# Kernel optimization log

Measured on AMD Instinct MI355X. Metric: run time of the kernel, lower is better.

The kernel has to match this reference:

```python
import jax, jax.numpy as jnp
import numpy as np

# --- config (matches init_kwargs) ---
HID = 2048      # hidden_size
H = 16          # num_attention_heads
D_NOPE = 128    # qk_nope_head_dim
D_ROPE = 64     # qk_rope_head_dim
D_Q = D_NOPE + D_ROPE  # 192
D_V = 128       # v_head_dim
QR = 1536       # q_lora_rank
KVR = 512       # kv_lora_rank
PH = 16         # pattern_heads
PD = HID // PH  # 128
THETA = 10000.0
EPS = 1e-6


def rmsnorm(x, w):
    var = jnp.mean(jnp.square(x), axis=-1, keepdims=True)
    return x * jax.lax.rsqrt(var + EPS) * w


def rope_cos_sin(seq_len):
    inv_freq = 1.0 / (THETA ** (jnp.arange(0, D_ROPE, 2, dtype=jnp.float32) / D_ROPE))
    t = jnp.arange(seq_len, dtype=jnp.float32)
    freqs = jnp.outer(t, inv_freq)            # [S, D_ROPE/2]
    emb = jnp.concatenate([freqs, freqs], -1)  # [S, D_ROPE]
    return jnp.cos(emb), jnp.sin(emb)


def rotate_half(x):
    x1, x2 = jnp.split(x, 2, axis=-1)
    return jnp.concatenate([-x2, x1], axis=-1)


def apply_rope(x, cos, sin):
    # x: [B, H, S, D_ROPE]; cos/sin: [S, D_ROPE]
    return x * cos[None, None] + rotate_half(x) * sin[None, None]


def setup_inputs() -> dict:
    key = jax.random.key(0)
    ks = jax.random.split(key, 12)
    def w(k, shape):
        return (jax.random.normal(k, shape, jnp.float32) / np.sqrt(shape[-1])).astype(jnp.float32)
    B, S = 2, 1024
    return {
        "hidden_states": jax.random.normal(ks[0], (B, S, HID), jnp.float32),
        "q_a_w": w(ks[1], (QR, HID)),
        "q_a_ln_w": jnp.ones((QR,), jnp.float32),
        "q_b_w": w(ks[2], (H * D_Q, QR)),
        "kv_a_w": w(ks[3], (KVR + H * D_ROPE, HID)),
        "kv_a_ln_w": jnp.ones((KVR,), jnp.float32),
        "kv_b_w": w(ks[4], (H * (D_NOPE + D_V), KVR)),
        "o_w": w(ks[5], (HID, H * D_V)),
        "sp_q_w": w(ks[6], (HID, HID)),
        "sp_k_w": w(ks[7], (HID, HID)),
        "sp_v_w": w(ks[8], (HID, HID)),
        "sp_o_w": w(ks[9], (HID, HID)),
        "gate_w": w(ks[10], (2, HID)),
        "gate_b": jnp.zeros((2,), jnp.float32),
    }


def reference(hidden_states, q_a_w, q_a_ln_w, q_b_w, kv_a_w, kv_a_ln_w, kv_b_w,
              o_w, sp_q_w, sp_k_w, sp_v_w, sp_o_w, gate_w, gate_b):
    b, s, _ = hidden_states.shape
    dt = hidden_states.dtype

    # ---- main MLA path ----
    q_mid = rmsnorm(hidden_states @ q_a_w.T, q_a_ln_w)                      # [B,S,QR]
    q = (q_mid @ q_b_w.T).reshape(b, s, H, D_Q).transpose(0, 2, 1, 3)       # [B,H,S,Dq]
    q_nope, q_pe = q[..., :D_NOPE], q[..., D_NOPE:]

    kv_a = hidden_states @ kv_a_w.T                                         # [B,S,KVR+H*Dr]
    kv_lora, k_pe_flat = kv_a[..., :KVR], kv_a[..., KVR:]
    k_pe = k_pe_flat.reshape(b, s, H, D_ROPE).transpose(0, 2, 1, 3)         # [B,H,S,Dr]

    kv = (rmsnorm(kv_lora, kv_a_ln_w) @ kv_b_w.T)
    kv = kv.reshape(b, s, H, D_NOPE + D_V).transpose(0, 2, 1, 3)            # [B,H,S,Dn+Dv]
    k_nope, v = kv[..., :D_NOPE], kv[..., D_NOPE:]

    cos, sin = rope_cos_sin(s)
    q_pe = apply_rope(q_pe, cos, sin)
    k_pe = apply_rope(k_pe, cos, sin)

    qf = jnp.concatenate([q_nope, q_pe], -1)                                # [B,H,S,Dq]
    kf = jnp.concatenate([k_nope, k_pe], -1)

    scale = D_Q ** -0.5
    scores = jnp.einsum('bhqd,bhkd->bhqk', qf, kf) * scale
    probs = jax.nn.softmax(scores.astype(jnp.float32), axis=-1).astype(dt)
    ctx = jnp.einsum('bhqk,bhkd->bhqd', probs, v)                           # [B,H,S,Dv]
    main_out = ctx.transpose(0, 2, 1, 3).reshape(b, s, H * D_V) @ o_w.T     # [B,S,HID]

    # ---- self pattern path (standard MHA on hidden_states) ----
    def split_heads(x):
        return x.reshape(b, s, PH, PD).transpose(0, 2, 1, 3)
    pq = split_heads(hidden_states @ sp_q_w.T)
    pk = split_heads(hidden_states @ sp_k_w.T)
    pv = split_heads(hidden_states @ sp_v_w.T)
    p_scores = jnp.einsum('bhqd,bhkd->bhqk', pq, pk) * (PD ** -0.5)
    p_probs = jax.nn.softmax(p_scores.astype(jnp.float32), axis=-1).astype(dt)
    p_ctx = jnp.einsum('bhqk,bhkd->bhqd', p_probs, pv)
    pattern_out = p_ctx.transpose(0, 2, 1, 3).reshape(b, s, HID) @ sp_o_w.T

    # ---- learned gate over paths ----
    gates = jax.nn.softmax(hidden_states @ gate_w.T + gate_b, axis=-1)      # [B,S,2]
    return gates[..., 0:1] * main_out + gates[..., 1:2] * pattern_out
```

## Files before the change

kernel.cpp:

```cpp
#include <hip/hip_runtime.h>
#include <math.h>
#include <stdint.h>

#define HIDN  2048
#define NH    16
#define DNOPE 128
#define DROPE 64
#define DQ    192
#define DV    128
#define QRANK 1536
#define KVRANK 512
#define SEQ   1024
#define NBATCH 2
#define NTOK  (NBATCH*SEQ)
#define EPSV  1e-6f

typedef unsigned short u16;
typedef unsigned int   u32;
typedef __attribute__((ext_vector_type(8))) short  short8;
typedef __attribute__((ext_vector_type(8))) unsigned short ushort8;
typedef __attribute__((ext_vector_type(4))) float  f32x4;

__device__ __forceinline__ u16 f2b(float f) {
    u32 u = __float_as_uint(f);
    u = (u + 0x7fffu + ((u >> 16) & 1u)) >> 16;
    return (u16)u;
}
__device__ __forceinline__ float b2f(u16 h) {
    return __uint_as_float(((u32)h) << 16);
}

__device__ __forceinline__ void async_copy16(const u16* g, u16* l) {
    __builtin_amdgcn_global_load_lds(
        (const __attribute__((address_space(1))) u32*)g,
        (__attribute__((address_space(3))) u32*)l,
        16, 0, 0);
}

__device__ __forceinline__ int swz(int r, int c) { return r * 4 + (c ^ ((r >> 1) & 3)); }

struct CastArgs {
    const float* s[10];
    u16* d[10];
    int cum[11];
};
__global__ __launch_bounds__(256)
void cast_all(CastArgs a, int total_chunks)
{
    int c = blockIdx.x * 256 + threadIdx.x;
    if (c >= total_chunks) return;
    int seg = 0;
    #pragma unroll
    for (int i = 1; i < 10; ++i) seg += (c >= a.cum[i]) ? 1 : 0;
    int local = c - a.cum[seg];
    const float* src = a.s[seg] + (size_t)local * 8;
    u16* dst = a.d[seg] + (size_t)local * 8;
    float4 x = *(const float4*)(src);
    float4 y = *(const float4*)(src + 4);
    ushort8 o;
    o[0]=f2b(x.x); o[1]=f2b(x.y); o[2]=f2b(x.z); o[3]=f2b(x.w);
    o[4]=f2b(y.x); o[5]=f2b(y.y); o[6]=f2b(y.z); o[7]=f2b(y.w);
    *(ushort8*)(dst) = o;
}

struct GemmSeg {
    const u16* X; const u16* W;
    float* Cf; u16* Cb; u16* Cb2; u16* Cb3;
    int K; int ldx; int ldc; int mode; int bx0;
};
struct GemmArgs { GemmSeg seg[3]; int nseg; };

__global__ __launch_bounds__(256)
void gemm_multi(GemmArgs a)
{
    __shared__ __align__(16) u16 As[2 * 4096];
    __shared__ __align__(16) u16 Bs[2 * 4096];
    int s = 0;
    if (a.nseg > 1 && (int)blockIdx.x >= a.seg[1].bx0) s = 1;
    if (a.nseg > 2 && (int)blockIdx.x >= a.seg[2].bx0) s = 2;
    const GemmSeg g = a.seg[s];

    const int tid = threadIdx.x;
    const int bn = ((int)blockIdx.x - g.bx0) * 128;
    const int bm = blockIdx.y * 128;
    const int lane = tid & 63, wv = tid >> 6;
    const int lm = lane & 15, lq = lane >> 4;
    const int wm = (wv >> 1) * 64, wn = (wv & 1) * 64;
    const int ldx = g.ldx, K = g.K;
    const u16* Xp = g.X;
    const u16* Wp = g.W;

    auto stage = [&](int kt, int buf) {
        int k0 = kt * 32;
        #pragma unroll
        for (int it = 0; it < 2; ++it) {
            int base = wv * 64 + it * 256;
            int slot = base + lane;
            int r = slot >> 2, c = (slot & 3) ^ ((r >> 1) & 3);
            async_copy16(Xp + (size_t)(bm + r) * ldx + k0 + c * 8,
                         As + buf * 4096 + base * 8);
            async_copy16(Wp + (size_t)(bn + r) * K + k0 + c * 8,
                         Bs + buf * 4096 + base * 8);
        }
    };

    f32x4 acc[4][4] = {};
    const int niter = K >> 5;
    stage(0, 0);
    for (int kt = 0; kt < niter; ++kt) {
        int cur = kt & 1;
        __syncthreads();
        if (kt + 1 < niter) stage(kt + 1, cur ^ 1);
        const u16* Ab = As + cur * 4096;
        const u16* Bb = Bs + cur * 4096;
        short8 af[4], bf[4];
        #pragma unroll
        for (int mt = 0; mt < 4; ++mt) {
            int R = wm + mt * 16 + lm;
            af[mt] = *(const short8*)(Ab + swz(R, lq) * 8);
        }
        #pragma unroll
        for (int nt = 0; nt < 4; ++nt) {
            int R = wn + nt * 16 + lm;
            bf[nt] = *(const short8*)(Bb + swz(R, lq) * 8);
        }
        #pragma unroll
        for (int mt = 0; mt < 4; ++mt)
            #pragma unroll
            for (int nt = 0; nt < 4; ++nt)
                acc[mt][nt] = __builtin_amdgcn_mfma_f32_16x16x32_bf16(
                    af[mt], bf[nt], acc[mt][nt], 0, 0, 0);
    }

    const int mode = g.mode;
    #pragma unroll
    for (int mt = 0; mt < 4; ++mt) {
        int token0 = bm + wm + mt * 16 + lq * 4;
        #pragma unroll
        for (int nt = 0; nt < 4; ++nt) {
            int feat = bn + wn + nt * 16 + lm;
            #pragma unroll
            for (int i = 0; i < 4; ++i) {
                float v = acc[mt][nt][i];
                int tok = token0 + i;
                int b2 = tok >> 10, s2 = tok & (SEQ - 1);
                if (mode == 0) {
                    g.Cf[(size_t)tok * g.ldc + feat] = v;
                } else if (mode == 5) {
                    g.Cb[(size_t)tok * g.ldc + feat] = f2b(v);
                } else if (mode == 1) {
                    int h2 = feat / DQ, d = feat - h2 * DQ;
                    g.Cb[((size_t)((b2 * NH + h2) * SEQ + s2)) * DQ + d] = f2b(v);
                } else if (mode == 3) {
                    int h2 = feat >> 8, c = feat & 255;
                    if (c < 128)
                        g.Cb[((size_t)((b2 * NH + h2) * SEQ + s2)) * DQ + c] = f2b(v);
                    else
                        g.Cb2[((size_t)((b2 * NH + h2) * 128 + (c - 128))) * SEQ + s2] = f2b(v);
                } else {
                    int wsel = feat >> 11;
                    int f2 = feat & 2047;
                    int h2 = f2 >> 7, d = f2 & 127;
                    if (wsel == 0)
                        g.Cb[((size_t)((b2 * NH + h2) * SEQ + s2)) * 128 + d] = f2b(v);
                    else if (wsel == 1)
                        g.Cb2[((size_t)((b2 * NH + h2) * SEQ + s2)) * 128 + d] = f2b(v);
                    else
                        g.Cb3[((size_t)((b2 * NH + h2) * 128 + d)) * SEQ + s2] = f2b(v);
                }
            }
        }
    }
}

__global__ __launch_bounds__(256)
void rmsnorm_fused(u16* __restrict__ amid, const float* __restrict__ qw,
                   const float* __restrict__ kvw)
{
    int row = blockIdx.x;
    u16* x; const float* w; int D;
    if (row < NTOK) { x = amid + (size_t)row * 3072;            w = qw;  D = QRANK; }
    else            { x = amid + (size_t)(row - NTOK) * 3072 + QRANK; w = kvw; D = KVRANK; }
    float ss = 0.f;
    for (int d = threadIdx.x; d < D; d += 256) { float v = b2f(x[d]); ss += v * v; }
    __shared__ float red[256];
    red[threadIdx.x] = ss;
    __syncthreads();
    for (int off = 128; off > 0; off >>= 1) {
        if (threadIdx.x < off) red[threadIdx.x] += red[threadIdx.x + off];
        __syncthreads();
    }
    float inv = rsqrtf(red[0] / (float)D + EPSV);
    for (int d = threadIdx.x; d < D; d += 256)
        x[d] = f2b(b2f(x[d]) * inv * w[d]);
}

__global__ __launch_bounds__(256)
void rope_fused(u16* __restrict__ qf, const u16* __restrict__ amid,
                u16* __restrict__ kf)
{
    int t = blockIdx.x * 256 + threadIdx.x;
    bool isq = t < (1 << 20);
    int tt = isq ? t : t - (1 << 20);
    int i = tt & 31, s = (tt >> 5) & (SEQ - 1), bh = tt >> 15;
    float inv_freq = powf(10000.f, -(float)i / 32.f);
    float ang = (float)s * inv_freq;
    float c, sn; sincosf(ang, &sn, &c);
    if (isq) {
        u16* p = qf + ((size_t)bh * SEQ + s) * DQ;
        float x1 = b2f(p[DNOPE + i]), x2 = b2f(p[DNOPE + 32 + i]);
        p[DNOPE + i]      = f2b(x1 * c - x2 * sn);
        p[DNOPE + 32 + i] = f2b(x2 * c + x1 * sn);
    } else {
        int h = bh & (NH - 1), bb = bh >> 4;
        const u16* src = amid + ((size_t)(bb * SEQ + s)) * 3072 + (QRANK + KVRANK) + h * DROPE;
        float x1 = b2f(src[i]), x2 = b2f(src[32 + i]);
        u16* dst = kf + ((size_t)bh * SEQ + s) * DQ + DNOPE;
        dst[i]      = f2b(x1 * c - x2 * sn);
        dst[32 + i] = f2b(x2 * c + x1 * sn);
    }
}

template<int DQK>
__device__ __forceinline__
void flash_body(const u16* __restrict__ Q, const u16* __restrict__ Kf,
                const u16* __restrict__ Vt, u16* __restrict__ ctx_out,
                float scale, u16* Ks, u16* Vs, u16* Ps, int qt, int h, int bb)
{
    constexpr int KSZ  = 32 * DQK;
    constexpr int VSZ  = 32 * 128;
    constexpr int NKIT = DQK / 64;
    constexpr int NT   = SEQ / 32;
    const int tid = threadIdx.x, lane = tid & 63, wv = tid >> 6;
    const int lm = lane & 15, lq = lane >> 4;
    const size_t bh = (size_t)bb * NH + h;
    const u16* Qb = Q + (bh * SEQ + qt * 64 + wv * 16) * (size_t)DQK;
    const u16* Kb = Kf + bh * SEQ * (size_t)DQK;
    const u16* Vb = Vt + bh * (size_t)128 * SEQ;

    short8 qfrag[DQK / 32];
    #pragma unroll
    for (int ks = 0; ks < DQK / 32; ++ks)
        qfrag[ks] = *(const short8*)(Qb + lm * DQK + ks * 32 + lq * 8);

    auto stage = [&](int kt, int buf) {
        #pragma unroll
        for (int it = 0; it < NKIT; ++it) {
            int base = it * 256 + wv * 64;
            int slot = base + lane;
            int plane = slot >> 7, rem = slot & 127;
            int key = rem >> 2, c = (rem & 3) ^ ((key >> 1) & 3);
            async_copy16(Kb + (size_t)(kt * 32 + key) * DQK + plane * 32 + c * 8,
                         Ks + buf * KSZ + base * 8);
        }
        #pragma unroll
        for (int it = 0; it < 2; ++it) {
            int base = it * 256 + wv * 64;
            int slot = base + lane;
            int d = slot >> 2, c = (slot & 3) ^ ((d >> 1) & 3);
            async_copy16(Vb + (size_t)d * SEQ + kt * 32 + c * 8,
                         Vs + buf * VSZ + base * 8);
        }
    };

    float m_i[4], l_i[4];
    #pragma unroll
    for (int i = 0; i < 4; ++i) { m_i[i] = -INFINITY; l_i[i] = 0.f; }
    f32x4 oacc[8] = {};

    stage(0, 0);
    for (int kt = 0; kt < NT; ++kt) {
        int cur = kt & 1;
        __syncthreads();
        if (kt + 1 < NT) stage(kt + 1, cur ^ 1);
        const u16* Kc = Ks + cur * KSZ;
        const u16* Vc = Vs + cur * VSZ;

        f32x4 sacc[2] = {};
        #pragma unroll
        for (int kb = 0; kb < 2; ++kb)
            #pragma unroll
            for (int ks = 0; ks < DQK / 32; ++ks) {
                int R = kb * 16 + lm;
                short8 kfr = *(const short8*)(Kc + ks * 1024 + swz(R, lq) * 8);
                sacc[kb] = __builtin_amdgcn_mfma_f32_16x16x32_bf16(
                    qfrag[ks], kfr, sacc[kb], 0, 0, 0);
            }

        float p0[4], p1[4], alpha[4];
        #pragma unroll
        for (int i = 0; i < 4; ++i) {
            float s0 = sacc[0][i] * scale, s1 = sacc[1][i] * scale;
            float mx = fmaxf(s0, s1);
            mx = fmaxf(mx, __shfl_xor(mx, 1));
            mx = fmaxf(mx, __shfl_xor(mx, 2));
            mx = fmaxf(mx, __shfl_xor(mx, 4));
            mx = fmaxf(mx, __shfl_xor(mx, 8));
            float mnew = fmaxf(m_i[i], mx);
            p0[i] = __expf(s0 - mnew);
            p1[i] = __expf(s1 - mnew);
            float sum = p0[i] + p1[i];
            sum += __shfl_xor(sum, 1);
            sum += __shfl_xor(sum, 2);
            sum += __shfl_xor(sum, 4);
            sum += __shfl_xor(sum, 8);
            alpha[i] = __expf(m_i[i] - mnew);
            l_i[i] = l_i[i] * alpha[i] + sum;
            m_i[i] = mnew;
        }

        u16* Pw = Ps + wv * 640;
        #pragma unroll
        for (int i = 0; i < 4; ++i) {
            Pw[(lq * 4 + i) * 40 + lm]      = f2b(p0[i]);
            Pw[(lq * 4 + i) * 40 + 16 + lm] = f2b(p1[i]);
        }
        short8 pfrag = *(const short8*)(Pw + lm * 40 + lq * 8);

        #pragma unroll
        for (int nt = 0; nt < 8; ++nt) {
            #pragma unroll
            for (int i = 0; i < 4; ++i) oacc[nt][i] *= alpha[i];
            int R = nt * 16 + lm;
            short8 vfr = *(const short8*)(Vc + swz(R, lq) * 8);
            oacc[nt] = __builtin_amdgcn_mfma_f32_16x16x32_bf16(
                pfrag, vfr, oacc[nt], 0, 0, 0);
        }
    }

    int s0 = qt * 64 + wv * 16 + lq * 4;
    #pragma unroll
    for (int i = 0; i < 4; ++i) {
        float inv = 1.f / l_i[i];
        u16* dst = ctx_out + ((size_t)(bb * SEQ + s0 + i) * NH + h) * 128;
        #pragma unroll
        for (int nt = 0; nt < 8; ++nt)
            dst[nt * 16 + lm] = f2b(oacc[nt][i] * inv);
    }
}

__global__ __launch_bounds__(256, 3)
void flash_fused(const u16* qf, const u16* kf, const u16* Vtg, u16* ctx,
                 const u16* pq, const u16* pk, const u16* pvt, u16* p_ctx,
                 float scale_main, float scale_pat)
{
    __shared__ __align__(16) u16 Ks[2 * 32 * DQ];
    __shared__ __align__(16) u16 Vs[2 * 32 * 128];
    __shared__ __align__(16) u16 Ps[4 * 16 * 40];
    int h = blockIdx.x, qtb = blockIdx.y, bb = blockIdx.z;
    if (qtb < 16)
        flash_body<DQ>(qf, kf, Vtg, ctx, scale_main, Ks, Vs, Ps, qtb, h, bb);
    else
        flash_body<128>(pq, pk, pvt, p_ctx, scale_pat, Ks, Vs, Ps, qtb - 16, h, bb);
}

__global__ __launch_bounds__(256)
void gate_combine(const float* __restrict__ x, const float* __restrict__ gw,
                  const float* __restrict__ gb,
                  const float* __restrict__ mo, const float* __restrict__ po,
                  float* __restrict__ out)
{
    const int tok = blockIdx.x;
    const float* xr = x + (size_t)tok * HIDN;
    float d0 = 0.f, d1 = 0.f;
    for (int i = threadIdx.x; i < HIDN; i += 256) {
        float v = xr[i];
        d0 += v * gw[i];
        d1 += v * gw[HIDN + i];
    }
    __shared__ float r0[256], r1[256];
    r0[threadIdx.x] = d0; r1[threadIdx.x] = d1;
    __syncthreads();
    for (int off = 128; off > 0; off >>= 1) {
        if (threadIdx.x < off) {
            r0[threadIdx.x] += r0[threadIdx.x + off];
            r1[threadIdx.x] += r1[threadIdx.x + off];
        }
        __syncthreads();
    }
    float l0 = r0[0] + gb[0], l1 = r1[0] + gb[1];
    float m = fmaxf(l0, l1);
    float e0 = __expf(l0 - m), e1 = __expf(l1 - m);
    float g0 = e0 / (e0 + e1), g1 = e1 / (e0 + e1);
    const float* mr = mo + (size_t)tok * HIDN;
    const float* pr = po + (size_t)tok * HIDN;
    float* orow = out + (size_t)tok * HIDN;
    for (int i = threadIdx.x; i < HIDN; i += 256)
        orow[i] = g0 * mr[i] + g1 * pr[i];
}

extern "C" void kernel_launch(void* const* d_in, const int* in_sizes, int n_in,
                              void* d_out, int out_size, void* d_ws, size_t ws_size,
                              hipStream_t stream)
{
    const float* X        = (const float*)d_in[0];
    const float* q_a_w    = (const float*)d_in[1];
    const float* q_a_ln_w = (const float*)d_in[2];
    const float* q_b_w    = (const float*)d_in[3];
    const float* kv_a_w   = (const float*)d_in[4];
    const float* kv_a_ln_w= (const float*)d_in[5];
    const float* kv_b_w   = (const float*)d_in[6];
    const float* o_w      = (const float*)d_in[7];
    const float* sp_q_w   = (const float*)d_in[8];
    const float* sp_k_w   = (const float*)d_in[9];
    const float* sp_v_w   = (const float*)d_in[10];
    const float* sp_o_w   = (const float*)d_in[11];
    const float* gate_w   = (const float*)d_in[12];
    const float* gate_b   = (const float*)d_in[13];
    float* out = (float*)d_out;

    char* p = (char*)d_ws;
    auto alloc = [&](size_t bytes) -> char* {
        char* r = p; p += (bytes + 255) & ~(size_t)255; return r;
    };
    u16* amid      = (u16*)alloc((size_t)NTOK * 3072 * 2);
    u16* Xb        = (u16*)alloc((size_t)NTOK * HIDN * 2);
    u16* aw_b      = (u16*)alloc((size_t)3072 * HIDN * 2);
    u16* q_b_wb    = (u16*)alloc((size_t)NH * DQ * QRANK * 2);
    u16* kv_b_wb   = (u16*)alloc((size_t)NH * 256 * KVRANK * 2);
    u16* o_wb      = (u16*)alloc((size_t)HIDN * HIDN * 2);
    u16* spqkv_wb  = (u16*)alloc((size_t)3 * HIDN * HIDN * 2);
    u16* sp_o_wb   = (u16*)alloc((size_t)HIDN * HIDN * 2);
    u16* qf        = (u16*)alloc((size_t)NTOK * NH * DQ * 2);
    u16* kf        = (u16*)alloc((size_t)NTOK * NH * DQ * 2);
    u16* Vtg       = (u16*)alloc((size_t)NBATCH * NH * 128 * SEQ * 2);
    u16* pq        = (u16*)alloc((size_t)NTOK * HIDN * 2);
    u16* pk        = (u16*)alloc((size_t)NTOK * HIDN * 2);
    u16* pvt    = aw_b;
    u16* ctx    = q_b_wb;
    u16* p_ctx  = spqkv_wb;
    float* patout = (float*)qf;

    dim3 blk(256);

    CastArgs ca;
    const float* srcs[10] = {X, q_a_w, kv_a_w, q_b_w, kv_b_w, o_w,
                             sp_q_w, sp_k_w, sp_v_w, sp_o_w};
    u16* dsts[10] = {Xb, aw_b, aw_b + (size_t)QRANK * HIDN, q_b_wb, kv_b_wb, o_wb,
                     spqkv_wb, spqkv_wb + (size_t)HIDN * HIDN,
                     spqkv_wb + (size_t)2 * HIDN * HIDN, sp_o_wb};
    int ns[10] = {NTOK * HIDN, QRANK * HIDN, 1536 * HIDN, NH * DQ * QRANK,
                  NH * 256 * KVRANK, HIDN * HIDN, HIDN * HIDN, HIDN * HIDN,
                  HIDN * HIDN, HIDN * HIDN};
    int cum = 0;
    for (int i = 0; i < 10; ++i) {
        ca.s[i] = srcs[i]; ca.d[i] = dsts[i];
        ca.cum[i] = cum; cum += ns[i] / 8;
    }
    ca.cum[10] = cum;
    cast_all<<<dim3((cum + 255) / 256), blk, 0, stream>>>(ca, cum);

    {
        GemmArgs ga = {};
        ga.nseg = 1;
        ga.seg[0] = {Xb, aw_b, nullptr, amid, nullptr, nullptr,
                     HIDN, HIDN, 3072, 5, 0};
        gemm_multi<<<dim3(24, 16), blk, 0, stream>>>(ga);
    }

    rmsnorm_fused<<<dim3(2 * NTOK), blk, 0, stream>>>(amid, q_a_ln_w, kv_a_ln_w);

    {
        GemmArgs ga = {};
        ga.nseg = 3;
        ga.seg[0] = {amid, q_b_wb, nullptr, qf, nullptr, nullptr,
                     QRANK, 3072, 0, 1, 0};
        ga.seg[1] = {amid + QRANK, kv_b_wb, nullptr, kf, Vtg, nullptr,
                     KVRANK, 3072, 0, 3, 24};
        ga.seg[2] = {Xb, spqkv_wb, nullptr, pq, pk, pvt,
                     HIDN, HIDN, 0, 4, 56};
        gemm_multi<<<dim3(104, 16), blk, 0, stream>>>(ga);
    }

    rope_fused<<<dim3(8192), blk, 0, stream>>>(qf, amid, kf);

    flash_fused<<<dim3(NH, 32, NBATCH), blk, 0, stream>>>(
        qf, kf, Vtg, ctx, pq, pk, pvt, p_ctx,
        1.0f / sqrtf((float)DQ), 1.0f / sqrtf(128.0f));

    {
        GemmArgs ga = {};
        ga.nseg = 2;
        ga.seg[0] = {ctx, o_wb, out, nullptr, nullptr, nullptr,
                     HIDN, HIDN, HIDN, 0, 0};
        ga.seg[1] = {p_ctx, sp_o_wb, patout, nullptr, nullptr, nullptr,
                     HIDN, HIDN, HIDN, 0, 16};
        gemm_multi<<<dim3(32, 16), blk, 0, stream>>>(ga);
    }

    gate_combine<<<dim3(NTOK), blk, 0, stream>>>(X, gate_w, gate_b, out, patout, out);
}
```

Measured before the change: 602.6 us.

## Enlarge GEMM tiles to 256x256 with 512 threads and four-stage async pipeline

Reworks the shared GEMM kernel to compute 256x256 output tiles with 8 waves, each wave owning a 128x64 sub-tile. The old double buffer becomes a four-stage LDS ring, paced by explicit vmcnt waits and raw barriers. Each k-step splits its MFMAs into two halves, with A and B prefetches interleaved between them and s_setprio raised around the MFMA blocks. The aim is more operand reuse per LDS load and better overlap of global loads with matrix math. In exchange it uses 128KB of LDS per block and launches far fewer blocks (96 for the first GEMM), which risks leaving many CUs idle.

```diff
diff --git a/kernel.cpp b/kernel.cpp
--- a/kernel.cpp
+++ b/kernel.cpp
@@ -70,71 +70,109 @@
 };
 struct GemmArgs { GemmSeg seg[3]; int nseg; };
 
-__global__ __launch_bounds__(256)
+__global__ __launch_bounds__(512, 2)
 void gemm_multi(GemmArgs a)
 {
-    __shared__ __align__(16) u16 As[2 * 4096];
-    __shared__ __align__(16) u16 Bs[2 * 4096];
+    __shared__ __align__(16) u16 As[4 * 8192];
+    __shared__ __align__(16) u16 Bs[4 * 8192];
     int s = 0;
     if (a.nseg > 1 && (int)blockIdx.x >= a.seg[1].bx0) s = 1;
     if (a.nseg > 2 && (int)blockIdx.x >= a.seg[2].bx0) s = 2;
     const GemmSeg g = a.seg[s];
 
     const int tid = threadIdx.x;
-    const int bn = ((int)blockIdx.x - g.bx0) * 128;
-    const int bm = blockIdx.y * 128;
+    const int bn = ((int)blockIdx.x - g.bx0) * 256;
+    const int bm = blockIdx.y * 256;
     const int lane = tid & 63, wv = tid >> 6;
     const int lm = lane & 15, lq = lane >> 4;
-    const int wm = (wv >> 1) * 64, wn = (wv & 1) * 64;
+    const int wm = (wv >> 2) * 128, wn = (wv & 3) * 64;
     const int ldx = g.ldx, K = g.K;
     const u16* Xp = g.X;
     const u16* Wp = g.W;
 
-    auto stage = [&](int kt, int buf) {
+    auto stageA = [&](int kt) {
+        int buf = kt & 3;
         int k0 = kt * 32;
         #pragma unroll
         for (int it = 0; it < 2; ++it) {
-            int base = wv * 64 + it * 256;
+            int base = it * 512 + wv * 64;
             int slot = base + lane;
             int r = slot >> 2, c = (slot & 3) ^ ((r >> 1) & 3);
             async_copy16(Xp + (size_t)(bm + r) * ldx + k0 + c * 8,
-                         As + buf * 4096 + base * 8);
+                         As + buf * 8192 + base * 8);
+        }
+    };
+    auto stageB = [&](int kt) {
+        int buf = kt & 3;
+        int k0 = kt * 32;
+        #pragma unroll
+        for (int it = 0; it < 2; ++it) {
+            int base = it * 512 + wv * 64;
+            int slot = base + lane;
+            int r = slot >> 2, c = (slot & 3) ^ ((r >> 1) & 3);
             async_copy16(Wp + (size_t)(bn + r) * K + k0 + c * 8,
-                         Bs + buf * 4096 + base * 8);
+                         Bs + buf * 8192 + base * 8);
         }
     };
 
-    f32x4 acc[4][4] = {};
+    f32x4 acc[8][4] = {};
     const int niter = K >> 5;
-    stage(0, 0);
+
+    stageA(0); stageB(0);
+    stageA(1); stageB(1);
+    stageA(2); stageB(2);
+
     for (int kt = 0; kt < niter; ++kt) {
-        int cur = kt & 1;
-        __syncthreads();
-        if (kt + 1 < niter) stage(kt + 1, cur ^ 1);
-        const u16* Ab = As + cur * 4096;
-        const u16* Bb = Bs + cur * 4096;
+        int rem = niter - kt;
+        if (rem > 2)       asm volatile("s_waitcnt vmcnt(8)" ::: "memory");
+        else if (rem == 2) asm volatile("s_waitcnt vmcnt(4)" ::: "memory");
+        else               asm volatile("s_waitcnt vmcnt(0)" ::: "memory");
+        __builtin_amdgcn_s_barrier();
+        __builtin_amdgcn_sched_barrier(0);
+
+        const u16* Ab = As + (kt & 3) * 8192;
+        const u16* Bb = Bs + (kt & 3) * 8192;
+        const bool more = (kt + 3) < niter;
+
+        if (more) stageA(kt + 3);
         short8 af[4], bf[4];
         #pragma unroll
-        for (int mt = 0; mt < 4; ++mt) {
-            int R = wm + mt * 16 + lm;
-            af[mt] = *(const short8*)(Ab + swz(R, lq) * 8);
-        }
-        #pragma unroll
-        for (int nt = 0; nt < 4; ++nt) {
-            int R = wn + nt * 16 + lm;
-            bf[nt] = *(const short8*)(Bb + swz(R, lq) * 8);
-        }
+        for (int mt = 0; mt < 4; ++mt)
+            af[mt] = *(const short8*)(Ab + swz(wm + mt * 16 + lm, lq) * 8);
+        #pragma unroll
+        for (int nt = 0; nt < 4; ++nt)
+            bf[nt] = *(const short8*)(Bb + swz(wn + nt * 16 + lm, lq) * 8);
+        asm volatile("s_waitcnt lgkmcnt(0)" ::: "memory");
+        __builtin_amdgcn_sched_barrier(0);
+        __builtin_amdgcn_s_setprio(1);
         #pragma unroll
         for (int mt = 0; mt < 4; ++mt)
             #pragma unroll
             for (int nt = 0; nt < 4; ++nt)
                 acc[mt][nt] = __builtin_amdgcn_mfma_f32_16x16x32_bf16(
                     af[mt], bf[nt], acc[mt][nt], 0, 0, 0);
+        __builtin_amdgcn_s_setprio(0);
+
+        if (more) stageB(kt + 3);
+        short8 af2[4];
+        #pragma unroll
+        for (int mt = 0; mt < 4; ++mt)
+            af2[mt] = *(const short8*)(Ab + swz(wm + 64 + mt * 16 + lm, lq) * 8);
+        asm volatile("s_waitcnt lgkmcnt(0)" ::: "memory");
+        __builtin_amdgcn_sched_barrier(0);
+        __builtin_amdgcn_s_setprio(1);
+        #pragma unroll
+        for (int mt = 0; mt < 4; ++mt)
+            #pragma unroll
+            for (int nt = 0; nt < 4; ++nt)
+                acc[4 + mt][nt] = __builtin_amdgcn_mfma_f32_16x16x32_bf16(
+                    af2[mt], bf[nt], acc[4 + mt][nt], 0, 0, 0);
+        __builtin_amdgcn_s_setprio(0);
     }
 
     const int mode = g.mode;
     #pragma unroll
-    for (int mt = 0; mt < 4; ++mt) {
+    for (int mt = 0; mt < 8; ++mt) {
         int token0 = bm + wm + mt * 16 + lq * 4;
         #pragma unroll
         for (int nt = 0; nt < 4; ++nt) {
@@ -432,6 +470,7 @@
     float* patout = (float*)qf;
 
     dim3 blk(256);
+    dim3 blkg(512);
 
     CastArgs ca;
     const float* srcs[10] = {X, q_a_w, kv_a_w, q_b_w, kv_b_w, o_w,
@@ -455,7 +494,7 @@
         ga.nseg = 1;
         ga.seg[0] = {Xb, aw_b, nullptr, amid, nullptr, nullptr,
                      HIDN, HIDN, 3072, 5, 0};
-        gemm_multi<<<dim3(24, 16), blk, 0, stream>>>(ga);
+        gemm_multi<<<dim3(12, 8), blkg, 0, stream>>>(ga);
     }
 
     rmsnorm_fused<<<dim3(2 * NTOK), blk, 0, stream>>>(amid, q_a_ln_w, kv_a_ln_w);
@@ -466,10 +505,10 @@
         ga.seg[0] = {amid, q_b_wb, nullptr, qf, nullptr, nullptr,
                      QRANK, 3072, 0, 1, 0};
         ga.seg[1] = {amid + QRANK, kv_b_wb, nullptr, kf, Vtg, nullptr,
-                     KVRANK, 3072, 0, 3, 24};
+                     KVRANK, 3072, 0, 3, 12};
         ga.seg[2] = {Xb, spqkv_wb, nullptr, pq, pk, pvt,
-                     HIDN, HIDN, 0, 4, 56};
-        gemm_multi<<<dim3(104, 16), blk, 0, stream>>>(ga);
+                     HIDN, HIDN, 0, 4, 28};
+        gemm_multi<<<dim3(52, 8), blkg, 0, stream>>>(ga);
     }
 
     rope_fused<<<dim3(8192), blk, 0, stream>>>(qf, amid, kf);
@@ -484,8 +523,8 @@
         ga.seg[0] = {ctx, o_wb, out, nullptr, nullptr, nullptr,
                      HIDN, HIDN, HIDN, 0, 0};
         ga.seg[1] = {p_ctx, sp_o_wb, patout, nullptr, nullptr, nullptr,
-                     HIDN, HIDN, HIDN, 0, 16};
-        gemm_multi<<<dim3(32, 16), blk, 0, stream>>>(ga);
+                     HIDN, HIDN, HIDN, 0, 8};
+        gemm_multi<<<dim3(16, 8), blkg, 0, stream>>>(ga);
     }
 
     gate_combine<<<dim3(NTOK), blk, 0, stream>>>(X, gate_w, gate_b, out, patout, out);
```

Result: slower. 787.3 us (+30.7%).
